# Kernel tuning notes

Hardware: AMD Instinct MI355X
Metric: run time of the kernel (lower is better)

Reference implementation:

```python
import jax, jax.numpy as jnp
import numpy as np

B, T, D = 4, 2048, 768
H, HD = 8, 96          # n_heads, head_dim
NB = HD // 24          # number of 24-dim Leech blocks per head
NEG_INF = -1e30


def _leech_kernel_24():
    # QR of the bidiagonal/circulant base matrix, as in generate_leech_kernel
    base = np.zeros((24, 24), dtype=np.float32)
    for i in range(23):
        base[i, i] = 2.0
        base[i, i + 1] = 2.0
    base[23, 23] = 2.0
    base[23, 0] = -2.0
    q, _ = np.linalg.qr(base)
    return jnp.asarray(q, dtype=jnp.float32)


def setup_inputs() -> dict:
    key = jax.random.key(0)
    k1, k2, k3 = jax.random.split(key, 3)
    x = jax.random.normal(k1, (B, T, D), dtype=jnp.float32)
    w_qkv = jax.random.normal(k2, (3 * D, D), dtype=jnp.float32) * (D ** -0.5)
    w_out = jax.random.normal(k3, (D, D), dtype=jnp.float32) * (D ** -0.5)
    kernel = _leech_kernel_24()
    return {"x": x, "w_qkv": w_qkv, "w_out": w_out, "kernel": kernel}


def reference(x, w_qkv, w_out, kernel):
    Bx, Tx, Dx = x.shape
    scale = HD ** -0.5
    # qkv projection (bias=False)
    qkv = jnp.einsum('btd,ed->bte', x, w_qkv)            # [B,T,3D]
    qkv = qkv.reshape(Bx, Tx, 3, H, HD).transpose(2, 0, 3, 1, 4)  # [3,B,H,T,HD]
    q, k, v = qkv[0], qkv[1], qkv[2]
    # per-24-block orthogonal Leech rotation on q and k
    q = jnp.einsum('bhtni,ij->bhtnj', q.reshape(Bx, H, Tx, NB, 24), kernel)
    k = jnp.einsum('bhtni,ij->bhtnj', k.reshape(Bx, H, Tx, NB, 24), kernel)
    q = q.reshape(Bx, H, Tx, HD)
    k = k.reshape(Bx, H, Tx, HD)
    # causal attention (manual softmax; dropout inactive in eval)
    scores = jnp.einsum('bhqd,bhkd->bhqk', q, k) * scale
    causal = jnp.tril(jnp.ones((Tx, Tx), dtype=bool))
    scores = jnp.where(causal[None, None], scores, NEG_INF)
    attn = jax.nn.softmax(scores, axis=-1)
    out = jnp.einsum('bhqk,bhkd->bhqd', attn, v)          # [B,H,T,HD]
    out = out.transpose(0, 2, 1, 3).reshape(Bx, Tx, Dx)
    return jnp.einsum('btd,ed->bte', out, w_out)
```

## Files before the change

### kernel.cpp

```cpp
#include <hip/hip_runtime.h>
#include <cstdint>
#include <cstddef>

#define Bq 4
#define T 2048
#define Dm 768
#define H 8
#define HD 96
#define BH 32
#define QEL ((size_t)BH*T*HD)
#define KEL ((size_t)BH*T*128)
#define PSTRIDE 98304
#define QS 0.14724703336f
#define KVB 64
#define M0 12.0f

typedef unsigned int u32;
typedef unsigned long long u64;
typedef _Float16 f16x8 __attribute__((ext_vector_type(8)));
typedef _Float16 f16x4 __attribute__((ext_vector_type(4)));
typedef float f32x4 __attribute__((ext_vector_type(4)));

__global__ __launch_bounds__(256)
void cvt_fused(const float* __restrict__ x, const float* __restrict__ wq,
               const float* __restrict__ wo, _Float16* __restrict__ xh,
               _Float16* __restrict__ wqh, _Float16* __restrict__ woh)
{
    const int tid  = threadIdx.x;
    const int lane = tid & 63;
    const int gw   = (blockIdx.x * 256 + tid) >> 6;
    const int kc   = gw % 96;
    const int grp  = gw / 96;

    const float* in;
    _Float16* out;
    int row;
    if (grp < 128)      { in = x;  out = xh;  row = grp * 64 + lane; }
    else if (grp < 164) { in = wq; out = wqh; row = (grp - 128) * 64 + lane; }
    else                { in = wo; out = woh; row = (grp - 164) * 64 + lane; }

    const float4 a = *reinterpret_cast<const float4*>(in + (size_t)row * 768 + kc * 8);
    const float4 b = *reinterpret_cast<const float4*>(in + (size_t)row * 768 + kc * 8 + 4);
    f16x8 h;
    h[0] = (_Float16)a.x; h[1] = (_Float16)a.y; h[2] = (_Float16)a.z; h[3] = (_Float16)a.w;
    h[4] = (_Float16)b.x; h[5] = (_Float16)b.y; h[6] = (_Float16)b.z; h[7] = (_Float16)b.w;
    *reinterpret_cast<f16x8*>(
        out + (size_t)(row >> 7) * PSTRIDE + (size_t)kc * 1024 + (row & 127) * 8) = h;
}

template <bool SCATTER>
__global__ __launch_bounds__(256)
void gemm_mfma(const _Float16* __restrict__ At, const _Float16* __restrict__ Bt,
               _Float16* __restrict__ qb, _Float16* __restrict__ kpd,
               _Float16* __restrict__ vtb, float* __restrict__ C,
               int N, int nx)
{
    constexpr int NSTEP = Dm / 32;
    __shared__ _Float16 As[2][4 * 128 * 8];
    __shared__ _Float16 Bs[2][4 * 128 * 8];

    const int tid  = threadIdx.x;
    const int lane = tid & 63;
    const int wid  = tid >> 6;
    const int li   = lane & 15;
    const int lg   = lane >> 4;
    const int wr   = wid >> 1;
    const int wc   = wid & 1;

    const int qch = gridDim.x >> 3;
    const int id  = (blockIdx.x & 7) * qch + (blockIdx.x >> 3);
    const int m0  = (id / nx) * 128;
    const int n0  = (id % nx) * 128;

    const _Float16* baseA = At + (size_t)(m0 >> 7) * PSTRIDE;
    const _Float16* baseB = Bt + (size_t)(n0 >> 7) * PSTRIDE;

    f32x4 acc[4][4];
#pragma unroll
    for (int i = 0; i < 4; ++i)
#pragma unroll
        for (int j = 0; j < 4; ++j) acc[i][j] = (f32x4)0.f;

    auto STAGE = [&](int t, int b) {
        const _Float16* pa = baseA + (t << 12);
        const _Float16* pb = baseB + (t << 12);
#pragma unroll
        for (int i = 0; i < 2; ++i) {
            const int s = wid * 64 + i * 256;
            __builtin_amdgcn_global_load_lds(
                (const __attribute__((address_space(1))) void*)(pa + (size_t)(s + lane) * 8),
                (__attribute__((address_space(3))) void*)&As[b][s * 8], 16, 0, 0);
            __builtin_amdgcn_global_load_lds(
                (const __attribute__((address_space(1))) void*)(pb + (size_t)(s + lane) * 8),
                (__attribute__((address_space(3))) void*)&Bs[b][s * 8], 16, 0, 0);
        }
    };

    STAGE(0, 0);
    asm volatile("s_waitcnt vmcnt(0)" ::: "memory");
    __builtin_amdgcn_s_barrier();

    for (int t = 0; t < NSTEP; ++t) {
        const int p = t & 1;
        if (t + 1 < NSTEP) STAGE(t + 1, p ^ 1);

        f16x8 af[4], bf[4];
#pragma unroll
        for (int i = 0; i < 4; ++i)
            af[i] = *reinterpret_cast<const f16x8*>(
                &As[p][(lg * 128 + wr * 64 + i * 16 + li) * 8]);
#pragma unroll
        for (int j = 0; j < 4; ++j)
            bf[j] = *reinterpret_cast<const f16x8*>(
                &Bs[p][(lg * 128 + wc * 64 + j * 16 + li) * 8]);
        asm volatile("s_waitcnt lgkmcnt(0)" ::: "memory");
#pragma unroll
        for (int i = 0; i < 4; ++i)
#pragma unroll
            for (int j = 0; j < 4; ++j)
                acc[i][j] = __builtin_amdgcn_mfma_f32_16x16x32_f16(
                    af[i], bf[j], acc[i][j], 0, 0, 0);

        asm volatile("s_waitcnt vmcnt(0) lgkmcnt(0)" ::: "memory");
        __builtin_amdgcn_s_barrier();
    }

#pragma unroll
    for (int i = 0; i < 4; ++i) {
#pragma unroll
        for (int r = 0; r < 4; ++r) {
            const int m = m0 + wr * 64 + i * 16 + lg * 4 + r;
            if (SCATTER) {
                const int b_ = m >> 11, t_ = m & 2047;
#pragma unroll
                for (int j = 0; j < 4; ++j) {
                    const int e = n0 + wc * 64 + j * 16 + li;
                    const int c = e / Dm;
                    const int rem = e - c * Dm;
                    const int h = rem / HD;
                    const int d = rem - h * HD;
                    const size_t bhx = (size_t)(b_ * H + h);
                    const float v = acc[i][j][r];
                    if (c == 0)
                        qb[(bhx * T + t_) * HD + d] = (_Float16)(v * QS);
                    else if (c == 1)
                        kpd[(bhx * T + t_) * 128 + d] = (_Float16)v;
                    else
                        vtb[(bhx * 96 + d) * T + t_] = (_Float16)v;
                }
            } else {
#pragma unroll
                for (int j = 0; j < 4; ++j) {
                    const int n = n0 + wc * 64 + j * 16 + li;
                    C[(size_t)m * N + n] = acc[i][j][r];
                }
            }
        }
    }
}

__global__ __launch_bounds__(256)
void attn_mfma(const _Float16* __restrict__ QG, const _Float16* __restrict__ KG,
               const _Float16* __restrict__ VtG, _Float16* __restrict__ aoh)
{
    __shared__ __align__(16) _Float16 Klds[2][64 * 128];
    __shared__ __align__(16) _Float16 Vlds[2][112 * 64];
    __shared__ __align__(16) _Float16 Pl[4][16][72];

    const int tid  = threadIdx.x;
    const int lane = tid & 63;
    const int wid  = tid >> 6;
    const int lg   = lane >> 4;
    const int li   = lane & 15;

    const int bh = blockIdx.x & 31;
    const int i  = blockIdx.x >> 5;
    const int qt0 = i, qt1 = 31 - i;

    {
        const u32 one2 = 0x3C003C00u;
        u32* vp0 = reinterpret_cast<u32*>(&Vlds[0][96 * 64]);
        u32* vp1 = reinterpret_cast<u32*>(&Vlds[1][96 * 64]);
#pragma unroll
        for (int k = tid; k < 512; k += 256) {
            const u32 v = (k < 32) ? one2 : 0u;
            vp0[k] = v; vp1[k] = v;
        }
    }
    __syncthreads();

    f16x8 qf0[3], qf1[3];
    {
        const _Float16* qr0 = QG + ((size_t)bh * T + qt0 * 64 + wid * 16 + li) * HD;
        const _Float16* qr1 = QG + ((size_t)bh * T + qt1 * 64 + wid * 16 + li) * HD;
#pragma unroll
        for (int ch = 0; ch < 3; ++ch) {
            qf0[ch] = *reinterpret_cast<const f16x8*>(qr0 + ch * 32 + lg * 8);
            qf1[ch] = *reinterpret_cast<const f16x8*>(qr1 + ch * 32 + lg * 8);
        }
    }

    const int swz = (li & 7) << 3;
    int kofs[4][3], vofs[7][2];
#pragma unroll
    for (int kt = 0; kt < 4; ++kt)
#pragma unroll
        for (int ch = 0; ch < 3; ++ch)
            kofs[kt][ch] = (kt * 16 + li) * 128 + ((ch * 32 + lg * 8) ^ swz);
#pragma unroll
    for (int dt = 0; dt < 7; ++dt)
#pragma unroll
        for (int pc = 0; pc < 2; ++pc)
            vofs[dt][pc] = (dt * 16 + li) * 64 + ((pc * 32 + lg * 8) ^ swz);

    const int rK = lane >> 4;
    const int cK = (lane & 15) * 8;
    const int rV = lane >> 3;
    const int cV = (lane & 7) * 8;
    auto STAGE = [&](int kb, int b) {
#pragma unroll
        for (int ii = 0; ii < 4; ++ii) {
            const int r  = wid * 16 + ii * 4 + rK;
            const int c0 = cK ^ (((ii * 4 + rK) & 7) << 3);
            const _Float16* src = KG + ((size_t)(bh * T + kb + r)) * 128 + c0;
            __builtin_amdgcn_global_load_lds(
                (const __attribute__((address_space(1))) void*)src,
                (__attribute__((address_space(3))) void*)&Klds[b][(wid * 16 + ii * 4) * 128],
                16, 0, 0);
        }
#pragma unroll
        for (int jj = 0; jj < 3; ++jj) {
            const int r  = wid * 24 + jj * 8 + rV;
            const int c0 = cV ^ (rV << 3);
            const _Float16* src = VtG + ((size_t)(bh * 96 + r)) * T + kb + c0;
            __builtin_amdgcn_global_load_lds(
                (const __attribute__((address_space(1))) void*)src,
                (__attribute__((address_space(3))) void*)&Vlds[b][(wid * 24 + jj * 8) * 64],
                16, 0, 0);
        }
    };

    f32x4 acc0[7], acc1[7];
#pragma unroll
    for (int dt = 0; dt < 7; ++dt) { acc0[dt] = (f32x4)0.f; acc1[dt] = (f32x4)0.f; }

    auto ROUND_FULL = [&](const f16x8 (&qf)[3], f32x4 (&acc)[7],
                          int p, int nextkb) {
        STAGE(nextkb, p ^ 1);
        asm volatile("s_waitcnt vmcnt(7)" ::: "memory");
        __builtin_amdgcn_s_barrier();

        const _Float16* Kb = &Klds[p][0];
        const _Float16* Vb = &Vlds[p][0];

        f16x8 kf[4][3];
#pragma unroll
        for (int kt = 0; kt < 4; ++kt)
#pragma unroll
            for (int ch = 0; ch < 3; ++ch)
                kf[kt][ch] = *reinterpret_cast<const f16x8*>(Kb + kofs[kt][ch]);

        f32x4 st[4];
        __builtin_amdgcn_s_setprio(1);
#pragma unroll
        for (int kt = 0; kt < 4; ++kt) {
            st[kt] = (f32x4)(-M0);
#pragma unroll
            for (int ch = 0; ch < 3; ++ch)
                st[kt] = __builtin_amdgcn_mfma_f32_16x16x32_f16(
                    kf[kt][ch], qf[ch], st[kt], 0, 0, 0);
        }
        __builtin_amdgcn_s_setprio(0);

#pragma unroll
        for (int kt = 0; kt < 4; ++kt) {
            const auto a = __builtin_amdgcn_cvt_pkrtz(
                __builtin_amdgcn_exp2f(st[kt][0]),
                __builtin_amdgcn_exp2f(st[kt][1]));
            const auto b = __builtin_amdgcn_cvt_pkrtz(
                __builtin_amdgcn_exp2f(st[kt][2]),
                __builtin_amdgcn_exp2f(st[kt][3]));
            const u64 w = (u64)__builtin_bit_cast(u32, a) |
                          ((u64)__builtin_bit_cast(u32, b) << 32);
            *reinterpret_cast<u64*>(&Pl[wid][li][kt * 16 + lg * 4]) = w;
        }

#pragma unroll
        for (int pc = 0; pc < 2; ++pc) {
            const f16x8 pf = *reinterpret_cast<const f16x8*>(
                &Pl[wid][li][pc * 32 + lg * 8]);
            __builtin_amdgcn_s_setprio(1);
#pragma unroll
            for (int dt = 0; dt < 7; ++dt) {
                const f16x8 vf = *reinterpret_cast<const f16x8*>(Vb + vofs[dt][pc]);
                acc[dt] = __builtin_amdgcn_mfma_f32_16x16x32_f16(
                    pf, vf, acc[dt], 0, 0, 0);
            }
            __builtin_amdgcn_s_setprio(0);
        }

        asm volatile("s_waitcnt lgkmcnt(0)" ::: "memory");
        __builtin_amdgcn_s_barrier();
    };

    auto ROUND_DIAG = [&](int kb, int q0w, const f16x8 (&qf)[3], f32x4 (&acc)[7],
                          int p, int nextkb, bool has_next) {
        if (has_next) {
            STAGE(nextkb, p ^ 1);
            asm volatile("s_waitcnt vmcnt(7)" ::: "memory");
        } else {
            asm volatile("s_waitcnt vmcnt(0)" ::: "memory");
        }
        __builtin_amdgcn_s_barrier();

        const _Float16* Kb = &Klds[p][0];
        const _Float16* Vb = &Vlds[p][0];
        const int nkt = min(4, ((q0w + 15 - kb) >> 4) + 1);

        f16x8 kf[4][3];
#pragma unroll
        for (int kt = 0; kt < 4; ++kt)
            if (kt < nkt) {
#pragma unroll
                for (int ch = 0; ch < 3; ++ch)
                    kf[kt][ch] = *reinterpret_cast<const f16x8*>(Kb + kofs[kt][ch]);
            }

        f32x4 st[4];
        __builtin_amdgcn_s_setprio(1);
#pragma unroll
        for (int kt = 0; kt < 4; ++kt) {
            st[kt] = (f32x4)(-M0);
            if (kt < nkt) {
#pragma unroll
                for (int ch = 0; ch < 3; ++ch)
                    st[kt] = __builtin_amdgcn_mfma_f32_16x16x32_f16(
                        kf[kt][ch], qf[ch], st[kt], 0, 0, 0);
            }
        }
        __builtin_amdgcn_s_setprio(0);

        const int qg = q0w + li;
#pragma unroll
        for (int kt = 0; kt < 4; ++kt)
            if (kt < nkt && kb + kt * 16 + 15 > q0w) {
#pragma unroll
                for (int rr = 0; rr < 4; ++rr) {
                    const int kg = kb + kt * 16 + lg * 4 + rr;
                    if (kg > qg) st[kt][rr] = -1e30f;
                }
            }

#pragma unroll
        for (int kt = 0; kt < 4; ++kt)
            if (kt < nkt) {
                const auto a = __builtin_amdgcn_cvt_pkrtz(
                    __builtin_amdgcn_exp2f(st[kt][0]),
                    __builtin_amdgcn_exp2f(st[kt][1]));
                const auto b = __builtin_amdgcn_cvt_pkrtz(
                    __builtin_amdgcn_exp2f(st[kt][2]),
                    __builtin_amdgcn_exp2f(st[kt][3]));
                const u64 w = (u64)__builtin_bit_cast(u32, a) |
                              ((u64)__builtin_bit_cast(u32, b) << 32);
                *reinterpret_cast<u64*>(&Pl[wid][li][kt * 16 + lg * 4]) = w;
            }
        if (nkt & 1)
            *reinterpret_cast<u64*>(&Pl[wid][li][nkt * 16 + lg * 4]) = 0ull;

        const int npc = (nkt + 1) >> 1;
#pragma unroll
        for (int pc = 0; pc < 2; ++pc)
            if (pc < npc) {
                const f16x8 pf = *reinterpret_cast<const f16x8*>(
                    &Pl[wid][li][pc * 32 + lg * 8]);
                __builtin_amdgcn_s_setprio(1);
#pragma unroll
                for (int dt = 0; dt < 7; ++dt) {
                    const f16x8 vf = *reinterpret_cast<const f16x8*>(Vb + vofs[dt][pc]);
                    acc[dt] = __builtin_amdgcn_mfma_f32_16x16x32_f16(
                        pf, vf, acc[dt], 0, 0, 0);
                }
                __builtin_amdgcn_s_setprio(0);
            }

        asm volatile("s_waitcnt lgkmcnt(0)" ::: "memory");
        __builtin_amdgcn_s_barrier();
    };

    STAGE(0, 0);
    const int q0w0 = qt0 * 64 + wid * 16;
    const int q0w1 = qt1 * 64 + wid * 16;
    int r = 0;
    for (int t = 0; t < i; ++t, ++r)
        ROUND_FULL(qf0, acc0, r & 1, (t + 1) * KVB);
    ROUND_DIAG(i * KVB, q0w0, qf0, acc0, r & 1, 0, true); ++r;
    for (int t = 0; t < 31 - i; ++t, ++r)
        ROUND_FULL(qf1, acc1, r & 1, (t + 1) * KVB);
    ROUND_DIAG((31 - i) * KVB, q0w1, qf1, acc1, r & 1, 0, false);

    const int ob = bh >> 3, oh = bh & 7;
#pragma unroll
    for (int rr = 0; rr < 4; ++rr) {
        {
            const float l    = __shfl(acc0[6][rr], lg << 4);
            const float linv = 1.0f / l;
            const int m = ob * T + qt0 * 64 + wid * 16 + lg * 4 + rr;
            _Float16* op = aoh + (size_t)(m >> 7) * PSTRIDE + (size_t)(m & 127) * 8
                         + (size_t)(oh * 12 + (li >> 3)) * 1024 + (li & 7);
#pragma unroll
            for (int dt = 0; dt < 6; ++dt)
                op[dt * 2048] = (_Float16)(acc0[dt][rr] * linv);
        }
        {
            const float l    = __shfl(acc1[6][rr], lg << 4);
            const float linv = 1.0f / l;
            const int m = ob * T + qt1 * 64 + wid * 16 + lg * 4 + rr;
            _Float16* op = aoh + (size_t)(m >> 7) * PSTRIDE + (size_t)(m & 127) * 8
                         + (size_t)(oh * 12 + (li >> 3)) * 1024 + (li & 7);
#pragma unroll
            for (int dt = 0; dt < 6; ++dt)
                op[dt * 2048] = (_Float16)(acc1[dt][rr] * linv);
        }
    }
}

extern "C" void kernel_launch(void* const* d_in, const int* in_sizes, int n_in,
                              void* d_out, int out_size, void* d_ws, size_t ws_size,
                              hipStream_t stream)
{
    const float* x     = (const float*)d_in[0];
    const float* w_qkv = (const float*)d_in[1];
    const float* w_out = (const float*)d_in[2];

    _Float16* qb  = (_Float16*)d_ws;
    _Float16* kpd = qb + QEL;
    _Float16* vtb = kpd + KEL;
    _Float16* aoh = vtb + QEL;
    _Float16* xh  = aoh + (size_t)Bq * T * Dm;
    _Float16* wqh = xh + (size_t)Bq * T * Dm;
    _Float16* woh = wqh + (size_t)3 * Dm * Dm;
    float* out = (float*)d_out;

    const int M = Bq * T;

    cvt_fused<<<dim3((128 + 36 + 12) * 96 / 4), dim3(256), 0, stream>>>(
        x, w_qkv, w_out, xh, wqh, woh);

    gemm_mfma<true><<<dim3((3 * Dm / 128) * (M / 128)), dim3(256), 0, stream>>>(
        xh, wqh, qb, kpd, vtb, nullptr, 3 * Dm, 3 * Dm / 128);

    attn_mfma<<<dim3(BH * (T / 128)), dim3(256), 0, stream>>>(qb, kpd, vtb, aoh);

    gemm_mfma<false><<<dim3((Dm / 128) * (M / 128)), dim3(256), 0, stream>>>(
        aoh, woh, nullptr, nullptr, nullptr, out, Dm, Dm / 128);
}
```

Baseline: 148.7 us.

## Load GEMM operands directly into registers instead of staging through LDS

Both projection GEMMs stop staging the A and B tiles through double-buffered shared memory with global_load_lds and barriers. Each wave now loads its own MFMA fragments straight from the pre-packed fp16 global layout into registers, double-buffered in registers across k-steps. This drops LDS traffic and block-wide barriers, but every fragment is fetched from global/L2 by both waves that share it, which roughly doubles global load traffic and raises register pressure.

After: 152.0 us. +2.2%, slower.

```diff
diff --git a/kernel.cpp b/kernel.cpp
--- a/kernel.cpp
+++ b/kernel.cpp
@@ -50,15 +50,11 @@
 
 template <bool SCATTER>
 __global__ __launch_bounds__(256)
-void gemm_mfma(const _Float16* __restrict__ At, const _Float16* __restrict__ Bt,
-               _Float16* __restrict__ qb, _Float16* __restrict__ kpd,
-               _Float16* __restrict__ vtb, float* __restrict__ C,
-               int N, int nx)
+void gemm_reg(const _Float16* __restrict__ At, const _Float16* __restrict__ Bt,
+              _Float16* __restrict__ qb, _Float16* __restrict__ kpd,
+              _Float16* __restrict__ vtb, float* __restrict__ C,
+              int N, int nx)
 {
-    constexpr int NSTEP = Dm / 32;
-    __shared__ _Float16 As[2][4 * 128 * 8];
-    __shared__ _Float16 Bs[2][4 * 128 * 8];
-
     const int tid  = threadIdx.x;
     const int lane = tid & 63;
     const int wid  = tid >> 6;
@@ -72,8 +68,10 @@
     const int m0  = (id / nx) * 128;
     const int n0  = (id % nx) * 128;
 
-    const _Float16* baseA = At + (size_t)(m0 >> 7) * PSTRIDE;
-    const _Float16* baseB = Bt + (size_t)(n0 >> 7) * PSTRIDE;
+    const _Float16* pa = At + (size_t)(m0 >> 7) * PSTRIDE
+                       + (size_t)lg * 1024 + (size_t)(wr * 64 + li) * 8;
+    const _Float16* pb = Bt + (size_t)(n0 >> 7) * PSTRIDE
+                       + (size_t)lg * 1024 + (size_t)(wc * 64 + li) * 8;
 
     f32x4 acc[4][4];
 #pragma unroll
@@ -81,49 +79,38 @@
 #pragma unroll
         for (int j = 0; j < 4; ++j) acc[i][j] = (f32x4)0.f;
 
-    auto STAGE = [&](int t, int b) {
-        const _Float16* pa = baseA + (t << 12);
-        const _Float16* pb = baseB + (t << 12);
-#pragma unroll
-        for (int i = 0; i < 2; ++i) {
-            const int s = wid * 64 + i * 256;
-            __builtin_amdgcn_global_load_lds(
-                (const __attribute__((address_space(1))) void*)(pa + (size_t)(s + lane) * 8),
-                (__attribute__((address_space(3))) void*)&As[b][s * 8], 16, 0, 0);
-            __builtin_amdgcn_global_load_lds(
-                (const __attribute__((address_space(1))) void*)(pb + (size_t)(s + lane) * 8),
-                (__attribute__((address_space(3))) void*)&Bs[b][s * 8], 16, 0, 0);
-        }
-    };
-
-    STAGE(0, 0);
-    asm volatile("s_waitcnt vmcnt(0)" ::: "memory");
-    __builtin_amdgcn_s_barrier();
-
-    for (int t = 0; t < NSTEP; ++t) {
-        const int p = t & 1;
-        if (t + 1 < NSTEP) STAGE(t + 1, p ^ 1);
-
-        f16x8 af[4], bf[4];
-#pragma unroll
-        for (int i = 0; i < 4; ++i)
-            af[i] = *reinterpret_cast<const f16x8*>(
-                &As[p][(lg * 128 + wr * 64 + i * 16 + li) * 8]);
-#pragma unroll
-        for (int j = 0; j < 4; ++j)
-            bf[j] = *reinterpret_cast<const f16x8*>(
-                &Bs[p][(lg * 128 + wc * 64 + j * 16 + li) * 8]);
-        asm volatile("s_waitcnt lgkmcnt(0)" ::: "memory");
-#pragma unroll
-        for (int i = 0; i < 4; ++i)
-#pragma unroll
-            for (int j = 0; j < 4; ++j)
-                acc[i][j] = __builtin_amdgcn_mfma_f32_16x16x32_f16(
-                    af[i], bf[j], acc[i][j], 0, 0, 0);
-
-        asm volatile("s_waitcnt vmcnt(0) lgkmcnt(0)" ::: "memory");
-        __builtin_amdgcn_s_barrier();
-    }
+    f16x8 a0[4], b0[4], a1[4], b1[4];
+
+#define LOADR(t, a, b)                                                        \
+    {                                                                         \
+        const _Float16* qa = pa + (size_t)(t) * 4096;                         \
+        const _Float16* qd = pb + (size_t)(t) * 4096;                         \
+        _Pragma("unroll")                                                     \
+        for (int i = 0; i < 4; ++i) {                                         \
+            a[i] = *reinterpret_cast<const f16x8*>(qa + i * 128);             \
+            b[i] = *reinterpret_cast<const f16x8*>(qd + i * 128);             \
+        }                                                                     \
+    }
+#define MFMAR(a, b)                                                           \
+    {                                                                         \
+        _Pragma("unroll")                                                     \
+        for (int i = 0; i < 4; ++i)                                           \
+            _Pragma("unroll")                                                 \
+            for (int j = 0; j < 4; ++j)                                       \
+                acc[i][j] = __builtin_amdgcn_mfma_f32_16x16x32_f16(           \
+                    a[i], b[j], acc[i][j], 0, 0, 0);                          \
+    }
+
+    LOADR(0, a0, b0);
+#pragma unroll
+    for (int t = 0; t < 24; t += 2) {
+        if (t + 1 < 24) LOADR(t + 1, a1, b1);
+        MFMAR(a0, b0);
+        if (t + 2 < 24) LOADR(t + 2, a0, b0);
+        MFMAR(a1, b1);
+    }
+#undef LOADR
+#undef MFMAR
 
 #pragma unroll
     for (int i = 0; i < 4; ++i) {
@@ -446,11 +433,11 @@
     cvt_fused<<<dim3((128 + 36 + 12) * 96 / 4), dim3(256), 0, stream>>>(
         x, w_qkv, w_out, xh, wqh, woh);
 
-    gemm_mfma<true><<<dim3((3 * Dm / 128) * (M / 128)), dim3(256), 0, stream>>>(
+    gemm_reg<true><<<dim3((3 * Dm / 128) * (M / 128)), dim3(256), 0, stream>>>(
         xh, wqh, qb, kpd, vtb, nullptr, 3 * Dm, 3 * Dm / 128);
 
     attn_mfma<<<dim3(BH * (T / 128)), dim3(256), 0, stream>>>(qb, kpd, vtb, aoh);
 
-    gemm_mfma<false><<<dim3((Dm / 128) * (M / 128)), dim3(256), 0, stream>>>(
+    gemm_reg<false><<<dim3((Dm / 128) * (M / 128)), dim3(256), 0, stream>>>(
         aoh, woh, nullptr, nullptr, nullptr, out, Dm, Dm / 128);
 }
```
